# Optimization experiments

Measured on AMD Instinct MI355X. Metric: run time of the kernel, lower is better.

Reference implementation:

```python
import jax, jax.numpy as jnp
import numpy as np

B, S, E = 16, 2048, 1024

def setup_inputs() -> dict:
    key = jax.random.key(0)
    ks = jax.random.split(key, 7)
    scale = 1.0 / np.sqrt(E)
    x = jax.random.normal(ks[0], (B, S, E), dtype=jnp.float32)
    wq = jax.random.normal(ks[1], (E, E), dtype=jnp.float32) * scale
    bq = jax.random.normal(ks[2], (E,), dtype=jnp.float32) * 0.01
    wk = jax.random.normal(ks[3], (E, E), dtype=jnp.float32) * scale
    bk = jax.random.normal(ks[4], (E,), dtype=jnp.float32) * 0.01
    wv = jax.random.normal(ks[5], (E, E), dtype=jnp.float32) * scale
    bv = jax.random.normal(ks[6], (E,), dtype=jnp.float32) * 0.01
    return {"x": x, "wq": wq, "bq": bq, "wk": wk, "bk": bk, "wv": wv, "bv": bv}

def reference(x, wq, bq, wk, bk, wv, bv):
    # Linear layers: y = x @ W^T + b (torch nn.Linear convention)
    Q = jnp.einsum('bse,fe->bsf', x, wq) + bq
    K = jnp.einsum('bse,fe->bsf', x, wk) + bk
    V = jnp.einsum('bse,fe->bsf', x, wv) + bv
    scale = 1.0 / jnp.sqrt(jnp.asarray(x.shape[-1], dtype=x.dtype))
    score = jnp.einsum('bqe,bke->bqk', Q, K) * scale  # [B,S,S]
    attn = jax.nn.softmax(score, axis=-1)
    # dropout is identity in eval mode
    context = jnp.einsum('bqk,bke->bqe', attn, V)  # [B,S,E]
    return jnp.mean(context, axis=1)  # [B,E]
```

## Files before the change

### kernel.cpp

```cpp
#include <hip/hip_runtime.h>


#define B_ 16
#define S_ 2048
#define E_ 1024

typedef __bf16 bf16x8 __attribute__((ext_vector_type(8)));
typedef float f32x4 __attribute__((ext_vector_type(4)));
typedef float f32x2 __attribute__((ext_vector_type(2)));

__device__ __forceinline__ unsigned short f2bf(float f) {
  unsigned int u = __float_as_uint(f);
  u = (u + 0x7FFFu + ((u >> 16) & 1u)) >> 16;
  return (unsigned short)u;
}

__global__ __launch_bounds__(256) void gvec_kernel(
    const float* __restrict__ wk, const float* __restrict__ bq,
    float* __restrict__ g) {
  const int e = blockIdx.x * 256 + threadIdx.x;
  const int f0 = blockIdx.y * 32;
  float acc = 0.f;
#pragma unroll
  for (int i = 0; i < 32; ++i) acc += wk[(size_t)(f0 + i) * E_ + e] * bq[f0 + i];
  atomicAdd(&g[e], acc);
}

__global__ __launch_bounds__(256) void cast_x_v_kernel(
    const float* __restrict__ x, const float* __restrict__ g,
    unsigned short* __restrict__ xbf, float* __restrict__ vs) {
  const int row = blockIdx.x, t = threadIdx.x;
  const size_t i = (size_t)row * E_ + t * 4;
  float4 v = *(const float4*)(x + i);
  float4 gv = *(const float4*)(g + t * 4);
  ushort4 o;
  o.x = f2bf(v.x); o.y = f2bf(v.y); o.z = f2bf(v.z); o.w = f2bf(v.w);
  *(ushort4*)(xbf + i) = o;
  float p = v.x * gv.x + v.y * gv.y + v.z * gv.z + v.w * gv.w;
#pragma unroll
  for (int off = 32; off >= 1; off >>= 1) p += __shfl_xor(p, off);
  __shared__ float wsp[4];
  if ((t & 63) == 0) wsp[t >> 6] = p;
  __syncthreads();
  if (t == 0) vs[row] = (wsp[0] + wsp[1] + wsp[2] + wsp[3]) * 0.03125f;
}

__global__ __launch_bounds__(256) void tcast_kernel(
    const float* __restrict__ src, unsigned short* __restrict__ dst) {
  __shared__ float tile[32][33];
  const int tx = threadIdx.x & 31, ty = threadIdx.x >> 5;
  const int f0 = blockIdx.y * 32, e0 = blockIdx.x * 32;
#pragma unroll
  for (int j = 0; j < 4; ++j)
    tile[ty + 8 * j][tx] = src[(size_t)(f0 + ty + 8 * j) * E_ + e0 + tx];
  __syncthreads();
#pragma unroll
  for (int j = 0; j < 4; ++j)
    dst[(size_t)(e0 + ty + 8 * j) * E_ + f0 + tx] = f2bf(tile[tx][ty + 8 * j]);
}

template <int MODE>
__global__ __launch_bounds__(256, 2) void gemm_bt(
    const unsigned short* __restrict__ A, const unsigned short* __restrict__ Bm,
    void* __restrict__ Cout, const float* __restrict__ vs,
    float* __restrict__ rowsum, float scale,
    int K, int lda, int ldb, int ldc,
    long long strideA, long long strideB, long long strideC) {
  __shared__ unsigned short As[128 * 64];
  __shared__ unsigned short Bs[128 * 64];

  const int tid = threadIdx.x;
  const int wave = tid >> 6;
  const int lane = tid & 63;
  const int bz = blockIdx.z;
  const unsigned short* Ab = A + (size_t)bz * strideA;
  const unsigned short* Bb = Bm + (size_t)bz * strideB;
  const int rowBase = blockIdx.y * 128;
  const int colBase = blockIdx.x * 128;

  const int waveM = wave >> 1, waveN = wave & 1;
  const int lrow = lane & 15, lq = lane >> 4;

  const int rsub = lane >> 3;
  const int gOff = (((lane & 7) ^ rsub) << 3);

  f32x4 acc[4][4];
#pragma unroll
  for (int i = 0; i < 4; ++i)
#pragma unroll
    for (int j = 0; j < 4; ++j) {
      f32x4 z = {0.f, 0.f, 0.f, 0.f};
      acc[i][j] = z;
    }

  for (int k0 = 0; k0 < K; k0 += 64) {
#pragma unroll
    for (int i = 0; i < 4; ++i) {
      const int chunk = wave * 4 + i;
      const int r = chunk * 8 + rsub;
      const unsigned short* ga = Ab + (size_t)(rowBase + r) * lda + (k0 + gOff);
      const unsigned short* gb = Bb + (size_t)(colBase + r) * ldb + (k0 + gOff);
      __builtin_amdgcn_global_load_lds(
          (const __attribute__((address_space(1))) void*)ga,
          (__attribute__((address_space(3))) void*)(&As[chunk * 512]), 16, 0, 0);
      __builtin_amdgcn_global_load_lds(
          (const __attribute__((address_space(1))) void*)gb,
          (__attribute__((address_space(3))) void*)(&Bs[chunk * 512]), 16, 0, 0);
    }
    __syncthreads();

#pragma unroll
    for (int ks = 0; ks < 2; ++ks) {
      const int gg = (((ks * 4 + lq) ^ (lrow & 7)) << 3);
      bf16x8 af[4], bfv[4];
#pragma unroll
      for (int mi = 0; mi < 4; ++mi)
        af[mi] = *(const bf16x8*)(&As[(waveM * 64 + mi * 16 + lrow) * 64 + gg]);
#pragma unroll
      for (int ni = 0; ni < 4; ++ni)
        bfv[ni] = *(const bf16x8*)(&Bs[(waveN * 64 + ni * 16 + lrow) * 64 + gg]);
#pragma unroll
      for (int mi = 0; mi < 4; ++mi)
#pragma unroll
        for (int ni = 0; ni < 4; ++ni)
          acc[mi][ni] = __builtin_amdgcn_mfma_f32_16x16x32_bf16(
              af[mi], bfv[ni], acc[mi][ni], 0, 0, 0);
    }
    __syncthreads();
  }

  if constexpr (MODE == 0) {
    unsigned short* Cb = (unsigned short*)Cout;
#pragma unroll
    for (int mi = 0; mi < 4; ++mi) {
      const int grow = rowBase + waveM * 64 + mi * 16 + lq * 4;
#pragma unroll
      for (int ni = 0; ni < 4; ++ni) {
        const int gcol = colBase + waveN * 64 + ni * 16 + lrow;
#pragma unroll
        for (int r = 0; r < 4; ++r)
          Cb[(size_t)(grow + r) * ldc + gcol] = f2bf(acc[mi][ni][r]);
      }
    }
  } else {
    unsigned char* Eb = (unsigned char*)Cout + (size_t)bz * strideC;
    float* rs = rowsum + (size_t)bz * S_;
    const float* vsb = vs + (size_t)bz * S_;
    float badd[4];
#pragma unroll
    for (int ni = 0; ni < 4; ++ni)
      badd[ni] = vsb[colBase + waveN * 64 + ni * 16 + lrow];
#pragma unroll
    for (int mi = 0; mi < 4; ++mi) {
      const int grow = rowBase + waveM * 64 + mi * 16 + lq * 4;
#pragma unroll
      for (int r = 0; r < 4; ++r) {
        float e[4];
        float partial = 0.f;
#pragma unroll
        for (int ni = 0; ni < 4; ++ni) {
          e[ni] = __expf(acc[mi][ni][r] * scale + badd[ni]);
          partial += e[ni];
        }
        unsigned int pk = 0;
        pk = __builtin_amdgcn_cvt_pk_fp8_f32(e[0], e[1], pk, false);
        pk = __builtin_amdgcn_cvt_pk_fp8_f32(e[2], e[3], pk, true);
        *(unsigned int*)(&Eb[(size_t)(grow + r) * S_ + colBase + waveN * 64 +
                             lrow * 4]) = pk;
        partial += __shfl_xor(partial, 1);
        partial += __shfl_xor(partial, 2);
        partial += __shfl_xor(partial, 4);
        partial += __shfl_xor(partial, 8);
        if (lrow == 0) atomicAdd(&rs[grow + r], partial);
      }
    }
  }
}

__global__ __launch_bounds__(256) void colsum_kernel(
    const unsigned int* __restrict__ Epk, const float* __restrict__ rowsum,
    float* __restrict__ wsum) {
  const int b = blockIdx.y, q0 = blockIdx.x * 64, t = threadIdx.x;
  __shared__ float rinv[64];
  if (t < 64) rinv[t] = 1.0f / rowsum[(size_t)b * S_ + q0 + t];
  __syncthreads();
  float cs[2][4] = {{0, 0, 0, 0}, {0, 0, 0, 0}};
  const unsigned int* Eb = Epk + ((size_t)b * S_ + q0) * (S_ / 4);
  for (int q = 0; q < 64; ++q) {
    const float rv = rinv[q];
    const unsigned int* row = Eb + (size_t)q * (S_ / 4);
#pragma unroll
    for (int j = 0; j < 2; ++j) {
      const unsigned int p = row[t + 256 * j];
      f32x2 lo = __builtin_amdgcn_cvt_pk_f32_fp8(p, false);
      f32x2 hi = __builtin_amdgcn_cvt_pk_f32_fp8(p, true);
      cs[j][0] += lo[0] * rv;
      cs[j][1] += lo[1] * rv;
      cs[j][2] += hi[0] * rv;
      cs[j][3] += hi[1] * rv;
    }
  }
  const float inv = 1.0f / (float)S_;
#pragma unroll
  for (int j = 0; j < 2; ++j) {
    const int d = t + 256 * j;
    const int base = (d >> 4) * 64 + (d & 15);
#pragma unroll
    for (int jj = 0; jj < 4; ++jj)
      atomicAdd(&wsum[(size_t)b * S_ + base + 16 * jj], cs[j][jj] * inv);
  }
}

__global__ __launch_bounds__(256) void xbar_kernel(
    const unsigned short* __restrict__ xbf, const float* __restrict__ wsum,
    float* __restrict__ xbar) {
  const int b = blockIdx.y, kc = blockIdx.x, t = threadIdx.x;
  float4 acc = {0.f, 0.f, 0.f, 0.f};
  for (int k0 = 0; k0 < 128; ++k0) {
    const int k = kc * 128 + k0;
    const float w = wsum[(size_t)b * S_ + k];
    const ushort4 xv =
        *(const ushort4*)(xbf + ((size_t)b * S_ + k) * E_ + t * 4);
    acc.x += w * __uint_as_float((unsigned int)xv.x << 16);
    acc.y += w * __uint_as_float((unsigned int)xv.y << 16);
    acc.z += w * __uint_as_float((unsigned int)xv.z << 16);
    acc.w += w * __uint_as_float((unsigned int)xv.w << 16);
  }
  float* xb = xbar + (size_t)b * E_ + t * 4;
  atomicAdd(&xb[0], acc.x);
  atomicAdd(&xb[1], acc.y);
  atomicAdd(&xb[2], acc.z);
  atomicAdd(&xb[3], acc.w);
}

__global__ __launch_bounds__(256) void out_kernel(
    const float* __restrict__ xbar, const float* __restrict__ wv,
    const float* __restrict__ bv, float* __restrict__ out) {
  const int gid = blockIdx.x * 256 + threadIdx.x;
  const int b = gid >> 10, e = gid & 1023;
  const int c0 = blockIdx.y * 64;
  const float4* xr = (const float4*)(xbar + (size_t)b * E_) + c0;
  const float4* wr = (const float4*)(wv + (size_t)e * E_) + c0;
  float s = 0.f;
  for (int j = 0; j < 64; ++j) {
    float4 a = xr[j], w = wr[j];
    s += a.x * w.x + a.y * w.y + a.z * w.z + a.w * w.w;
  }
  if (blockIdx.y == 0) s += bv[e];
  atomicAdd(&out[gid], s);
}

extern "C" void kernel_launch(void* const* d_in, const int* in_sizes, int n_in,
                              void* d_out, int out_size, void* d_ws,
                              size_t ws_size, hipStream_t stream) {
  const float* x = (const float*)d_in[0];
  const float* wq = (const float*)d_in[1];
  const float* bq = (const float*)d_in[2];
  const float* wk = (const float*)d_in[3];
  const float* wv = (const float*)d_in[5];
  const float* bv = (const float*)d_in[6];
  float* out = (float*)d_out;

  char* ws = (char*)d_ws;
  const size_t MB = 1ull << 20;
  unsigned short* xbf = (unsigned short*)(ws);
  unsigned short* y = (unsigned short*)(ws + 64 * MB);
  unsigned char* Ebuf = (unsigned char*)(ws + 128 * MB);
  unsigned short* WqT = (unsigned short*)(ws + 192 * MB);
  unsigned short* WkT = (unsigned short*)(ws + 194 * MB);
  unsigned short* Mt = (unsigned short*)(ws + 196 * MB);
  float* g = (float*)(ws + 198 * MB);
  float* rowsum = g + E_;
  float* wsum = rowsum + B_ * S_;
  float* xbar = wsum + B_ * S_;
  float* vs = xbar + B_ * E_;

  hipMemsetAsync(g, 0, (size_t)(E_ + 2 * B_ * S_ + B_ * E_) * sizeof(float),
                 stream);
  hipMemsetAsync(out, 0, (size_t)B_ * E_ * sizeof(float), stream);

  gvec_kernel<<<dim3(E_ / 256, 32), 256, 0, stream>>>(wk, bq, g);
  cast_x_v_kernel<<<B_ * S_, 256, 0, stream>>>(x, g, xbf, vs);
  tcast_kernel<<<dim3(32, 32), 256, 0, stream>>>(wq, WqT);
  tcast_kernel<<<dim3(32, 32), 256, 0, stream>>>(wk, WkT);

  gemm_bt<0><<<dim3(8, 8), 256, 0, stream>>>(
      WkT, WqT, (void*)Mt, nullptr, nullptr, 1.0f, E_, E_, E_, E_, 0, 0, 0);
  gemm_bt<0><<<dim3(E_ / 128, (B_ * S_) / 128), 256, 0, stream>>>(
      xbf, Mt, (void*)y, nullptr, nullptr, 1.0f, E_, E_, E_, E_, 0, 0, 0);
  gemm_bt<1><<<dim3(S_ / 128, S_ / 128, B_), 256, 0, stream>>>(
      y, xbf, (void*)Ebuf, vs, rowsum, 0.03125f, E_, E_, E_, S_,
      (long long)S_ * E_, (long long)S_ * E_, (long long)S_ * S_);

  colsum_kernel<<<dim3(S_ / 64, B_), 256, 0, stream>>>(
      (const unsigned int*)Ebuf, rowsum, wsum);
  xbar_kernel<<<dim3(16, B_), 256, 0, stream>>>(xbf, wsum, xbar);
  out_kernel<<<dim3(B_ * E_ / 256, 4), 256, 0, stream>>>(xbar, wv, bv, out);
}
```

Measured before the change: 490.9 us.

## Add 256x256-tile 8-wave GEMM with async LDS loads for the two big GEMMs

Adds a new gemm256 kernel with 256x256 output tiles, 8 waves per block, double-buffered 128 KB dynamic LDS filled by global_load_lds direct copies with XOR swizzling, and MFMA phases interleaved with staged loads and setprio hints. It replaces the 128x128 gemm_bt for the x·M projection and for the batched score GEMM with its fused exp/fp8 epilogue. The larger tiles raise arithmetic intensity and cut global traffic, and the explicit pipeline is meant to overlap loads with compute. In exchange it needs heavy register use (launch_bounds 512,2) and 128 KB LDS per block, which limits occupancy, and it relies on hand-written waitcnt counts being correct.

Result: faster. 480.0 us (-2.2%).

```diff
diff --git a/kernel.cpp b/kernel.cpp
--- a/kernel.cpp
+++ b/kernel.cpp
@@ -142,6 +142,195 @@
           Cb[(size_t)(grow + r) * ldc + gcol] = f2bf(acc[mi][ni][r]);
       }
     }
+  }
+}
+
+template <int MODE>
+__global__ __launch_bounds__(512, 2) void gemm256(
+    const unsigned short* __restrict__ A, const unsigned short* __restrict__ Bm,
+    void* __restrict__ Cout, const float* __restrict__ vs,
+    float* __restrict__ rowsum, float scale, int ldc,
+    long long strideA, long long strideB, long long strideC) {
+  extern __shared__ __align__(16) unsigned short lds[];
+  const int tid = threadIdx.x;
+  const int wave = tid >> 6;
+  const int lane = tid & 63;
+  const int waveM = wave >> 2, waveN = wave & 3;
+  const int lrow = lane & 15, lq = lane >> 4;
+  const int bz = blockIdx.z;
+  const int rowBase = blockIdx.y * 256;
+  const int colBase = blockIdx.x * 256;
+  const unsigned short* Ab = A + (size_t)bz * strideA;
+  const unsigned short* Bb = Bm + (size_t)bz * strideB;
+
+  const int rsub = lane >> 3;
+  const int gsw = ((lane & 7) ^ rsub) << 3;
+  const unsigned short* Ag =
+      Ab + (size_t)(rowBase + wave * 8 + rsub) * E_ + gsw;
+  const unsigned short* Bg =
+      Bb + (size_t)(colBase + (wave >> 2) * 64 + (wave & 3) * 8 + rsub) * E_ + gsw;
+  const int ALo = wave * 512;
+  const int BLo = (wave >> 2) * 4096 + (wave & 3) * 512;
+
+#define STG(gp, lo)                                             \
+  __builtin_amdgcn_global_load_lds(                             \
+      (const __attribute__((address_space(1))) void*)(gp),      \
+      (__attribute__((address_space(3))) void*)(lds + (lo)), 16, 0, 0)
+#define STG_A0(ko, q)                                   \
+  do {                                                  \
+    STG(Ag + (ko), (q) * 16384 + ALo);                  \
+    STG(Ag + (ko) + 131072, (q) * 16384 + ALo + 8192);  \
+  } while (0)
+#define STG_A1(ko, q)                                   \
+  do {                                                  \
+    STG(Ag + (ko) + 65536, (q) * 16384 + ALo + 4096);   \
+    STG(Ag + (ko) + 196608, (q) * 16384 + ALo + 12288); \
+  } while (0)
+#define STG_B0(ko, q)                                            \
+  do {                                                           \
+    STG(Bg + (ko), 32768 + (q) * 16384 + BLo);                   \
+    STG(Bg + (ko) + 131072, 32768 + (q) * 16384 + BLo + 8192);   \
+  } while (0)
+#define STG_B1(ko, q)                                            \
+  do {                                                           \
+    STG(Bg + (ko) + 32768, 32768 + (q) * 16384 + BLo + 2048);    \
+    STG(Bg + (ko) + 163840, 32768 + (q) * 16384 + BLo + 10240);  \
+  } while (0)
+
+  f32x4 acc[8][4];
+#pragma unroll
+  for (int i = 0; i < 8; ++i)
+#pragma unroll
+    for (int j = 0; j < 4; ++j) {
+      f32x4 z = {0.f, 0.f, 0.f, 0.f};
+      acc[i][j] = z;
+    }
+
+  STG_A0(0, 0); STG_B0(0, 0); STG_B1(0, 0); STG_A1(0, 0);
+  STG_A0(64, 1); STG_B0(64, 1); STG_B1(64, 1); STG_A1(64, 1);
+  asm volatile("s_waitcnt vmcnt(8)" ::: "memory");
+  __builtin_amdgcn_s_barrier();
+
+  const int rowA = (waveM * 128 + lrow) * 64;
+  const int rowB = (waveN * 64 + lrow) * 64;
+  const int g0 = (lq ^ (lrow & 7)) * 8;
+  const int g1 = ((4 | lq) ^ (lrow & 7)) * 8;
+
+  bf16x8 a[4][2], b0[2][2], b1[2][2];
+
+#pragma unroll 2
+  for (int t = 0; t < 16; ++t) {
+    const int q = t & 1;
+    const unsigned short* At = lds + q * 16384;
+    const unsigned short* Bt = lds + 32768 + q * 16384;
+    const int ko = t * 64 + 128;
+    const bool st = (t < 14);
+
+#pragma unroll
+    for (int mi = 0; mi < 4; ++mi) {
+      a[mi][0] = *(const bf16x8*)(At + rowA + mi * 1024 + g0);
+      a[mi][1] = *(const bf16x8*)(At + rowA + mi * 1024 + g1);
+    }
+#pragma unroll
+    for (int ni = 0; ni < 2; ++ni) {
+      b0[ni][0] = *(const bf16x8*)(Bt + rowB + ni * 1024 + g0);
+      b0[ni][1] = *(const bf16x8*)(Bt + rowB + ni * 1024 + g1);
+    }
+    __builtin_amdgcn_s_barrier();
+    asm volatile("s_waitcnt lgkmcnt(0)" ::: "memory");
+    __builtin_amdgcn_s_setprio(1);
+#pragma unroll
+    for (int mi = 0; mi < 4; ++mi)
+#pragma unroll
+      for (int ni = 0; ni < 2; ++ni) {
+        acc[mi][ni] = __builtin_amdgcn_mfma_f32_16x16x32_bf16(
+            a[mi][0], b0[ni][0], acc[mi][ni], 0, 0, 0);
+        acc[mi][ni] = __builtin_amdgcn_mfma_f32_16x16x32_bf16(
+            a[mi][1], b0[ni][1], acc[mi][ni], 0, 0, 0);
+      }
+    __builtin_amdgcn_s_setprio(0);
+    __builtin_amdgcn_s_barrier();
+
+#pragma unroll
+    for (int ni = 0; ni < 2; ++ni) {
+      b1[ni][0] = *(const bf16x8*)(Bt + rowB + (ni + 2) * 1024 + g0);
+      b1[ni][1] = *(const bf16x8*)(Bt + rowB + (ni + 2) * 1024 + g1);
+    }
+    if (st) STG_A0(ko, q);
+    __builtin_amdgcn_s_barrier();
+    asm volatile("s_waitcnt lgkmcnt(0)" ::: "memory");
+    __builtin_amdgcn_s_setprio(1);
+#pragma unroll
+    for (int mi = 0; mi < 4; ++mi)
+#pragma unroll
+      for (int ni = 0; ni < 2; ++ni) {
+        acc[mi][ni + 2] = __builtin_amdgcn_mfma_f32_16x16x32_bf16(
+            a[mi][0], b1[ni][0], acc[mi][ni + 2], 0, 0, 0);
+        acc[mi][ni + 2] = __builtin_amdgcn_mfma_f32_16x16x32_bf16(
+            a[mi][1], b1[ni][1], acc[mi][ni + 2], 0, 0, 0);
+      }
+    __builtin_amdgcn_s_setprio(0);
+    __builtin_amdgcn_s_barrier();
+
+#pragma unroll
+    for (int mi = 0; mi < 4; ++mi) {
+      a[mi][0] = *(const bf16x8*)(At + rowA + (mi + 4) * 1024 + g0);
+      a[mi][1] = *(const bf16x8*)(At + rowA + (mi + 4) * 1024 + g1);
+    }
+    if (st) STG_B0(ko, q);
+    __builtin_amdgcn_s_barrier();
+    asm volatile("s_waitcnt lgkmcnt(0)" ::: "memory");
+    __builtin_amdgcn_s_setprio(1);
+#pragma unroll
+    for (int mi = 0; mi < 4; ++mi)
+#pragma unroll
+      for (int ni = 0; ni < 2; ++ni) {
+        acc[mi + 4][ni + 2] = __builtin_amdgcn_mfma_f32_16x16x32_bf16(
+            a[mi][0], b1[ni][0], acc[mi + 4][ni + 2], 0, 0, 0);
+        acc[mi + 4][ni + 2] = __builtin_amdgcn_mfma_f32_16x16x32_bf16(
+            a[mi][1], b1[ni][1], acc[mi + 4][ni + 2], 0, 0, 0);
+      }
+    __builtin_amdgcn_s_setprio(0);
+    __builtin_amdgcn_s_barrier();
+
+    if (st) { STG_B1(ko, q); STG_A1(ko, q); }
+    __builtin_amdgcn_s_barrier();
+    __builtin_amdgcn_s_setprio(1);
+#pragma unroll
+    for (int mi = 0; mi < 4; ++mi)
+#pragma unroll
+      for (int ni = 0; ni < 2; ++ni) {
+        acc[mi + 4][ni] = __builtin_amdgcn_mfma_f32_16x16x32_bf16(
+            a[mi][0], b0[ni][0], acc[mi + 4][ni], 0, 0, 0);
+        acc[mi + 4][ni] = __builtin_amdgcn_mfma_f32_16x16x32_bf16(
+            a[mi][1], b0[ni][1], acc[mi + 4][ni], 0, 0, 0);
+      }
+    __builtin_amdgcn_s_setprio(0);
+    if (st)
+      asm volatile("s_waitcnt vmcnt(8)" ::: "memory");
+    else
+      asm volatile("s_waitcnt vmcnt(0)" ::: "memory");
+    __builtin_amdgcn_s_barrier();
+  }
+#undef STG_B1
+#undef STG_B0
+#undef STG_A1
+#undef STG_A0
+#undef STG
+
+  if constexpr (MODE == 0) {
+    unsigned short* Cb = (unsigned short*)Cout;
+#pragma unroll
+    for (int mi = 0; mi < 8; ++mi) {
+      const int grow = rowBase + waveM * 128 + mi * 16 + lq * 4;
+#pragma unroll
+      for (int ni = 0; ni < 4; ++ni) {
+        const int gcol = colBase + waveN * 64 + ni * 16 + lrow;
+#pragma unroll
+        for (int r = 0; r < 4; ++r)
+          Cb[(size_t)(grow + r) * ldc + gcol] = f2bf(acc[mi][ni][r]);
+      }
+    }
   } else {
     unsigned char* Eb = (unsigned char*)Cout + (size_t)bz * strideC;
     float* rs = rowsum + (size_t)bz * S_;
@@ -151,8 +340,8 @@
     for (int ni = 0; ni < 4; ++ni)
       badd[ni] = vsb[colBase + waveN * 64 + ni * 16 + lrow];
 #pragma unroll
-    for (int mi = 0; mi < 4; ++mi) {
-      const int grow = rowBase + waveM * 64 + mi * 16 + lq * 4;
+    for (int mi = 0; mi < 8; ++mi) {
+      const int grow = rowBase + waveM * 128 + mi * 16 + lq * 4;
 #pragma unroll
       for (int r = 0; r < 4; ++r) {
         float e[4];
@@ -275,6 +464,11 @@
   float* xbar = wsum + B_ * S_;
   float* vs = xbar + B_ * E_;
 
+  hipFuncSetAttribute(reinterpret_cast<const void*>(gemm256<0>),
+                      hipFuncAttributeMaxDynamicSharedMemorySize, 131072);
+  hipFuncSetAttribute(reinterpret_cast<const void*>(gemm256<1>),
+                      hipFuncAttributeMaxDynamicSharedMemorySize, 131072);
+
   hipMemsetAsync(g, 0, (size_t)(E_ + 2 * B_ * S_ + B_ * E_) * sizeof(float),
                  stream);
   hipMemsetAsync(out, 0, (size_t)B_ * E_ * sizeof(float), stream);
@@ -286,10 +480,10 @@
 
   gemm_bt<0><<<dim3(8, 8), 256, 0, stream>>>(
       WkT, WqT, (void*)Mt, nullptr, nullptr, 1.0f, E_, E_, E_, E_, 0, 0, 0);
-  gemm_bt<0><<<dim3(E_ / 128, (B_ * S_) / 128), 256, 0, stream>>>(
-      xbf, Mt, (void*)y, nullptr, nullptr, 1.0f, E_, E_, E_, E_, 0, 0, 0);
-  gemm_bt<1><<<dim3(S_ / 128, S_ / 128, B_), 256, 0, stream>>>(
-      y, xbf, (void*)Ebuf, vs, rowsum, 0.03125f, E_, E_, E_, S_,
+  gemm256<0><<<dim3(E_ / 256, (B_ * S_) / 256), 512, 131072, stream>>>(
+      xbf, Mt, (void*)y, nullptr, nullptr, 1.0f, E_, 0, 0, 0);
+  gemm256<1><<<dim3(S_ / 256, S_ / 256, B_), 512, 131072, stream>>>(
+      y, xbf, (void*)Ebuf, vs, rowsum, 0.03125f, S_,
       (long long)S_ * E_, (long long)S_ * E_, (long long)S_ * S_);
 
   colsum_kernel<<<dim3(S_ / 64, B_), 256, 0, stream>>>(
```

## Overlap next-tile global loads with MFMA and remap workgroups across XCDs

Applied to the files above, without the earlier changes.

Each k-iteration now reads the whole LDS tile into registers, synchronizes, then issues the global-to-LDS loads for the next tile while the MFMAs run on the register copies. The goal is to hide global load latency behind compute within a single LDS buffer. It also remaps the linear workgroup id so consecutive tiles land on the same XCD (8-way interleave), which should improve L2 reuse. In exchange, register pressure rises from holding both k-slices of fragments, and the remap assumes the workgroup count divides by 8.

Measured after the change: 565.8 us. 1.15x slower.

```diff
diff --git a/kernel.cpp b/kernel.cpp
--- a/kernel.cpp
+++ b/kernel.cpp
@@ -72,11 +72,21 @@
   const int tid = threadIdx.x;
   const int wave = tid >> 6;
   const int lane = tid & 63;
-  const int bz = blockIdx.z;
+
+  const unsigned nwg = gridDim.x * gridDim.y * gridDim.z;
+  const unsigned lin =
+      blockIdx.x + gridDim.x * (blockIdx.y + gridDim.y * blockIdx.z);
+  const unsigned cpx = nwg >> 3;
+  const unsigned tz = (lin & 7) * cpx + (lin >> 3);
+  const unsigned bxi = tz % gridDim.x;
+  const unsigned rest = tz / gridDim.x;
+  const unsigned byi = rest % gridDim.y;
+  const unsigned bz = rest / gridDim.y;
+
   const unsigned short* Ab = A + (size_t)bz * strideA;
   const unsigned short* Bb = Bm + (size_t)bz * strideB;
-  const int rowBase = blockIdx.y * 128;
-  const int colBase = blockIdx.x * 128;
+  const int rowBase = byi * 128;
+  const int colBase = bxi * 128;
 
   const int waveM = wave >> 1, waveN = wave & 1;
   const int lrow = lane & 15, lq = lane >> 4;
@@ -93,13 +103,13 @@
       acc[i][j] = z;
     }
 
-  for (int k0 = 0; k0 < K; k0 += 64) {
+  auto stage = [&](int kk) {
 #pragma unroll
     for (int i = 0; i < 4; ++i) {
       const int chunk = wave * 4 + i;
       const int r = chunk * 8 + rsub;
-      const unsigned short* ga = Ab + (size_t)(rowBase + r) * lda + (k0 + gOff);
-      const unsigned short* gb = Bb + (size_t)(colBase + r) * ldb + (k0 + gOff);
+      const unsigned short* ga = Ab + (size_t)(rowBase + r) * lda + (kk + gOff);
+      const unsigned short* gb = Bb + (size_t)(colBase + r) * ldb + (kk + gOff);
       __builtin_amdgcn_global_load_lds(
           (const __attribute__((address_space(1))) void*)ga,
           (__attribute__((address_space(3))) void*)(&As[chunk * 512]), 16, 0, 0);
@@ -107,26 +117,40 @@
           (const __attribute__((address_space(1))) void*)gb,
           (__attribute__((address_space(3))) void*)(&Bs[chunk * 512]), 16, 0, 0);
     }
-    __syncthreads();
-
+  };
+
+  stage(0);
+  asm volatile("s_waitcnt vmcnt(0)" ::: "memory");
+  __builtin_amdgcn_s_barrier();
+
+  for (int k0 = 0; k0 < K; k0 += 64) {
+    bf16x8 af[4][2], bfv[4][2];
 #pragma unroll
     for (int ks = 0; ks < 2; ++ks) {
       const int gg = (((ks * 4 + lq) ^ (lrow & 7)) << 3);
-      bf16x8 af[4], bfv[4];
 #pragma unroll
       for (int mi = 0; mi < 4; ++mi)
-        af[mi] = *(const bf16x8*)(&As[(waveM * 64 + mi * 16 + lrow) * 64 + gg]);
+        af[mi][ks] =
+            *(const bf16x8*)(&As[(waveM * 64 + mi * 16 + lrow) * 64 + gg]);
 #pragma unroll
       for (int ni = 0; ni < 4; ++ni)
-        bfv[ni] = *(const bf16x8*)(&Bs[(waveN * 64 + ni * 16 + lrow) * 64 + gg]);
+        bfv[ni][ks] =
+            *(const bf16x8*)(&Bs[(waveN * 64 + ni * 16 + lrow) * 64 + gg]);
+    }
+    asm volatile("s_waitcnt lgkmcnt(0)" ::: "memory");
+    __builtin_amdgcn_s_barrier();
+
+    if (k0 + 64 < K) stage(k0 + 64);
+#pragma unroll
+    for (int ks = 0; ks < 2; ++ks)
 #pragma unroll
       for (int mi = 0; mi < 4; ++mi)
 #pragma unroll
         for (int ni = 0; ni < 4; ++ni)
           acc[mi][ni] = __builtin_amdgcn_mfma_f32_16x16x32_bf16(
-              af[mi], bfv[ni], acc[mi][ni], 0, 0, 0);
-    }
-    __syncthreads();
+              af[mi][ks], bfv[ni][ks], acc[mi][ni], 0, 0, 0);
+    asm volatile("s_waitcnt vmcnt(0)" ::: "memory");
+    __builtin_amdgcn_s_barrier();
   }
 
   if constexpr (MODE == 0) {
```
